# Optimization experiments

Measured on AMD Instinct MI355X. Metric: run time of the kernel, lower is better.

The kernel has to match this reference:

```python
import jax, jax.numpy as jnp
import numpy as np

KH, KW = 3, 3
STRIDE, PAD, DIL = 1, 1, 1


def _unfold(x, kh, kw, stride, pad, dil):
    # torch.nn.functional.unfold equivalent: [B,C,H,W] -> [B, C*kh*kw, L]
    # conv_general_dilated_patches flattens feature dim in (C, kh, kw) order,
    # which matches torch unfold's channel-major ordering.
    p = jax.lax.conv_general_dilated_patches(
        x,
        filter_shape=(kh, kw),
        window_strides=(stride, stride),
        padding=[(pad, pad), (pad, pad)],
        rhs_dilation=(dil, dil),
    )  # [B, C*kh*kw, Ho, Wo]
    b, ck, ho, wo = p.shape
    return p.reshape(b, ck, ho * wo)


def setup_inputs() -> dict:
    key = jax.random.key(0)
    k1, k2, k3 = jax.random.split(key, 3)
    B, C, H, W_sp = 4, 8, 128, 128
    N, K = 8, KH * KW
    array = jax.random.normal(k1, (B, C, H, W_sp), dtype=jnp.float32)
    W = jax.random.normal(k2, (N, C, K, 1), dtype=jnp.float32)
    Bbias = jax.random.normal(k3, (N, C, 1, 1), dtype=jnp.float32)
    return {"array": array, "W": W, "Bbias": Bbias}


def reference(array, W, Bbias):
    Bn, C, H, W_sp = array.shape
    N, _, K, _ = W.shape
    # unfold -> [B, 1, C, K, L]  (matches torch reshape + unsqueeze(1))
    patches = _unfold(array, KH, KW, STRIDE, PAD, DIL).reshape(Bn, 1, C, K, -1)
    L = patches.shape[-1]
    mul = patches * W[None]                         # [B, N, C, K, L]
    size = jnp.sum(W, axis=2, keepdims=True)        # [N, C, 1, 1] (sum over K)
    mean = jnp.mean(mul, axis=3, keepdims=True)     # [B, N, C, 1, L]
    i = (mul - mean) ** 2 / size + Bbias[None]      # weighted variance + bias
    return i.reshape(Bn, -1, L)                     # [B, N*C*K, L]
```

## Files before the change

kernel.cpp:

```cpp
#include <hip/hip_runtime.h>


#define BB 4
#define NN 8
#define CC 8
#define KK 9
#define HH 128
#define WW 128
#define LL (HH * WW)

typedef float vf4 __attribute__((ext_vector_type(4)));

__global__ __launch_bounds__(256) void tvar_kernel(
    const float* __restrict__ arr,
    const float* __restrict__ Wt,
    const float* __restrict__ Bb,
    float* __restrict__ out)
{
    const int bid = blockIdx.x;
    const int hi = bid & 15;
    const int c  = (bid >> 4) & 7;
    const int n  = (bid >> 7) & 7;
    const int b  = bid >> 10;

    const int lt = threadIdx.x;
    const int w4 = lt & 31;
    const int h  = (hi << 3) | (lt >> 5);

    const float* wrow = Wt + (n * CC + c) * KK;
    float w9[KK];
    float wsum = 0.f;
    #pragma unroll
    for (int k = 0; k < KK; ++k) { w9[k] = wrow[k]; wsum += w9[k]; }
    const float sinv = 1.0f / wsum;
    const float bias = Bb[n * CC + c];

    const int ws = w4 << 2;
    const float* abase = arr + (size_t)((b * CC + c) * HH) * WW;
    float p[3][6];
    #pragma unroll
    for (int r = 0; r < 3; ++r) {
        const int hh = h + r - 1;
        if (hh >= 0 && hh < HH) {
            const float* row = abase + hh * WW + ws;
            const float4 v = *(const float4*)row;
            p[r][1] = v.x; p[r][2] = v.y; p[r][3] = v.z; p[r][4] = v.w;
            p[r][0] = (ws > 0)      ? row[-1] : 0.f;
            p[r][5] = (ws + 4 < WW) ? row[4]  : 0.f;
        } else {
            #pragma unroll
            for (int j = 0; j < 6; ++j) p[r][j] = 0.f;
        }
    }

    const float inv9 = 1.0f / 9.0f;
    float mean[4] = {0.f, 0.f, 0.f, 0.f};
    #pragma unroll
    for (int k = 0; k < KK; ++k) {
        const int kh = k / 3, kw = k - kh * 3;
        #pragma unroll
        for (int j = 0; j < 4; ++j)
            mean[j] += p[kh][j + kw] * w9[k];
    }
    #pragma unroll
    for (int j = 0; j < 4; ++j) mean[j] *= inv9;

    float* onb = out + (size_t)b * (NN * CC * KK) * LL
                     + (size_t)((n * CC + c) * KK) * LL
                     + (size_t)(h * WW + ws);
    #pragma unroll
    for (int k = 0; k < KK; ++k) {
        const int kh = k / 3, kw = k - kh * 3;
        vf4 o;
        #pragma unroll
        for (int j = 0; j < 4; ++j) {
            const float v = p[kh][j + kw] * w9[k];
            const float d = v - mean[j];
            o[j] = d * d * sinv + bias;
        }
        *(vf4*)(onb + (size_t)k * LL) = o;
    }
}

extern "C" void kernel_launch(void* const* d_in, const int* in_sizes, int n_in,
                              void* d_out, int out_size, void* d_ws, size_t ws_size,
                              hipStream_t stream) {
    const float* arr = (const float*)d_in[0];
    const float* Wt  = (const float*)d_in[1];
    const float* Bb  = (const float*)d_in[2];
    float* out = (float*)d_out;

    const int threads = 256;
    const int blocks = BB * NN * CC * 16;
    tvar_kernel<<<blocks, threads, 0, stream>>>(arr, Wt, Bb, out);
}
```

Measured before the change: 154.4 us.

## Assign one output plane per block and loop over rows

Remaps the grid so each block handles one (b, n*c, k) output plane and loops over all 128 rows. Each block now writes a single contiguous 64KB region rather than nine strided planes, which should give more sequential write streams. In exchange, every block reloads the input patches and recomputes the mean that the old kernel shared across all nine k values. Input reads and mean arithmetic therefore grow ninefold, though the input is small and likely stays in cache.

```diff
diff --git a/kernel.cpp b/kernel.cpp
--- a/kernel.cpp
+++ b/kernel.cpp
@@ -17,68 +17,67 @@
     const float* __restrict__ Bb,
     float* __restrict__ out)
 {
-    const int bid = blockIdx.x;
-    const int hi = bid & 15;
-    const int c  = (bid >> 4) & 7;
-    const int n  = (bid >> 7) & 7;
-    const int b  = bid >> 10;
+    const int k  = blockIdx.x;
+    const int nc = blockIdx.y;
+    const int b  = blockIdx.z;
+    const int c  = nc & 7;
 
-    const int lt = threadIdx.x;
-    const int w4 = lt & 31;
-    const int h  = (hi << 3) | (lt >> 5);
+    const int t  = threadIdx.x;
+    const int w4 = t & 31;
+    const int hb = t >> 5;
+    const int ws = w4 << 2;
 
-    const float* wrow = Wt + (n * CC + c) * KK;
+    const float* wrow = Wt + nc * KK;
     float w9[KK];
     float wsum = 0.f;
     #pragma unroll
-    for (int k = 0; k < KK; ++k) { w9[k] = wrow[k]; wsum += w9[k]; }
+    for (int kk = 0; kk < KK; ++kk) { w9[kk] = wrow[kk]; wsum += w9[kk]; }
     const float sinv = 1.0f / wsum;
-    const float bias = Bb[n * CC + c];
+    const float bias = Bb[nc];
+    const float wk   = w9[k];
+    const int kh = k / 3, kw = k - kh * 3;
+    const float inv9 = 1.0f / 9.0f;
 
-    const int ws = w4 << 2;
     const float* abase = arr + (size_t)((b * CC + c) * HH) * WW;
-    float p[3][6];
-    #pragma unroll
-    for (int r = 0; r < 3; ++r) {
-        const int hh = h + r - 1;
-        if (hh >= 0 && hh < HH) {
-            const float* row = abase + hh * WW + ws;
-            const float4 v = *(const float4*)row;
-            p[r][1] = v.x; p[r][2] = v.y; p[r][3] = v.z; p[r][4] = v.w;
-            p[r][0] = (ws > 0)      ? row[-1] : 0.f;
-            p[r][5] = (ws + 4 < WW) ? row[4]  : 0.f;
-        } else {
+    float* oplane = out + ((size_t)(b * (NN * CC) + nc) * KK + k) * LL;
+
+    #pragma unroll 2
+    for (int i = 0; i < 16; ++i) {
+        const int h = (i << 3) | hb;
+
+        float p[3][6];
+        #pragma unroll
+        for (int r = 0; r < 3; ++r) {
+            const int hh = h + r - 1;
+            if (hh >= 0 && hh < HH) {
+                const float* row = abase + hh * WW + ws;
+                const float4 v = *(const float4*)row;
+                p[r][1] = v.x; p[r][2] = v.y; p[r][3] = v.z; p[r][4] = v.w;
+                p[r][0] = (ws > 0)      ? row[-1] : 0.f;
+                p[r][5] = (ws + 4 < WW) ? row[4]  : 0.f;
+            } else {
+                #pragma unroll
+                for (int j = 0; j < 6; ++j) p[r][j] = 0.f;
+            }
+        }
+
+        float mean[4] = {0.f, 0.f, 0.f, 0.f};
+        #pragma unroll
+        for (int kk = 0; kk < KK; ++kk) {
+            const int rh = kk / 3, rw = kk - rh * 3;
             #pragma unroll
-            for (int j = 0; j < 6; ++j) p[r][j] = 0.f;
+            for (int j = 0; j < 4; ++j)
+                mean[j] += p[rh][j + rw] * w9[kk];
         }
-    }
 
-    const float inv9 = 1.0f / 9.0f;
-    float mean[4] = {0.f, 0.f, 0.f, 0.f};
-    #pragma unroll
-    for (int k = 0; k < KK; ++k) {
-        const int kh = k / 3, kw = k - kh * 3;
-        #pragma unroll
-        for (int j = 0; j < 4; ++j)
-            mean[j] += p[kh][j + kw] * w9[k];
-    }
-    #pragma unroll
-    for (int j = 0; j < 4; ++j) mean[j] *= inv9;
-
-    float* onb = out + (size_t)b * (NN * CC * KK) * LL
-                     + (size_t)((n * CC + c) * KK) * LL
-                     + (size_t)(h * WW + ws);
-    #pragma unroll
-    for (int k = 0; k < KK; ++k) {
-        const int kh = k / 3, kw = k - kh * 3;
         vf4 o;
         #pragma unroll
         for (int j = 0; j < 4; ++j) {
-            const float v = p[kh][j + kw] * w9[k];
-            const float d = v - mean[j];
+            const float v = p[kh][j + kw] * wk;
+            const float d = v - mean[j] * inv9;
             o[j] = d * d * sinv + bias;
         }
-        *(vf4*)(onb + (size_t)k * LL) = o;
+        *(vf4*)(oplane + h * WW + ws) = o;
     }
 }
 
@@ -90,7 +89,6 @@
     const float* Bb  = (const float*)d_in[2];
     float* out = (float*)d_out;
 
-    const int threads = 256;
-    const int blocks = BB * NN * CC * 16;
-    tvar_kernel<<<blocks, threads, 0, stream>>>(arr, Wt, Bb, out);
+    dim3 grid(KK, NN * CC, BB);
+    tvar_kernel<<<grid, 256, 0, stream>>>(arr, Wt, Bb, out);
 }
```

Measured after the change: 317.3 us. 105% more time.
